# Kernel tuning notes

Measured on AMD Instinct MI355X. Metric: run time of the kernel, lower is better.

## Reference

```python
import jax, jax.numpy as jnp
import numpy as np

N_NODES = 50000
N_EDGES = 800000
IN_DIM = 128
HID = 64
HEADS = 2
OUT_DIM = 2
N_GRAPHS = 512
NEG_SLOPE = 0.2


def setup_inputs() -> dict:
    key = jax.random.key(0)
    ks = jax.random.split(key, 16)
    x = jax.random.normal(ks[0], (N_NODES, IN_DIM), dtype=jnp.float32)
    edge_index = jax.random.randint(ks[1], (2, N_EDGES), 0, N_NODES, dtype=jnp.int64)
    batch = jnp.sort(jax.random.randint(ks[2], (N_NODES,), 0, N_GRAPHS, dtype=jnp.int64))
    s = 0.1
    W1 = jax.random.normal(ks[3], (IN_DIM, HEADS * HID), dtype=jnp.float32) * s
    a_src1 = jax.random.normal(ks[4], (HEADS, HID), dtype=jnp.float32) * s
    a_dst1 = jax.random.normal(ks[5], (HEADS, HID), dtype=jnp.float32) * s
    b1 = jnp.zeros((HEADS * HID,), dtype=jnp.float32)
    W2 = jax.random.normal(ks[6], (HEADS * HID, HID), dtype=jnp.float32) * s
    a_src2 = jax.random.normal(ks[7], (1, HID), dtype=jnp.float32) * s
    a_dst2 = jax.random.normal(ks[8], (1, HID), dtype=jnp.float32) * s
    b2 = jnp.zeros((HID,), dtype=jnp.float32)
    fcW = jax.random.normal(ks[9], (HID, OUT_DIM), dtype=jnp.float32) * s
    fcb = jnp.zeros((OUT_DIM,), dtype=jnp.float32)
    return dict(x=x, edge_index=edge_index, batch=batch,
                W1=W1, a_src1=a_src1, a_dst1=a_dst1, b1=b1,
                W2=W2, a_src2=a_src2, a_dst2=a_dst2, b2=b2,
                fcW=fcW, fcb=fcb)


def gat_layer(x, src, dst, W, a_src, a_dst, b, heads, c_out):
    # x: [N, F] -> h: [N, H, C]
    N = x.shape[0]
    h = (x @ W).reshape(N, heads, c_out)
    alpha_s = jnp.sum(h * a_src, axis=-1)  # [N, H]
    alpha_d = jnp.sum(h * a_dst, axis=-1)  # [N, H]
    e = jax.nn.leaky_relu(alpha_s[src] + alpha_d[dst], NEG_SLOPE)  # [E, H]
    # segment softmax over destination nodes
    emax = jax.ops.segment_max(e, dst, num_segments=N)  # [N, H]
    ex = jnp.exp(e - emax[dst])
    denom = jax.ops.segment_sum(ex, dst, num_segments=N)  # [N, H]
    coef = ex / denom[dst]  # [E, H]
    msg = h[src] * coef[..., None]  # [E, H, C]
    out = jax.ops.segment_sum(msg, dst, num_segments=N)  # [N, H, C]
    return out.reshape(N, heads * c_out) + b


def reference(x, edge_index, batch, W1, a_src1, a_dst1, b1, W2, a_src2, a_dst2, b2, fcW, fcb):
    N = x.shape[0]
    # PyG GATConv add_self_loops=True (shared graph for both layers)
    loops = jnp.arange(N, dtype=edge_index.dtype)
    src = jnp.concatenate([edge_index[0], loops])
    dst = jnp.concatenate([edge_index[1], loops])
    h = jax.nn.relu(gat_layer(x, src, dst, W1, a_src1, a_dst1, b1, HEADS, HID))
    h = jax.nn.relu(gat_layer(h, src, dst, W2, a_src2, a_dst2, b2, 1, HID))
    # global mean pool over graphs
    sums = jax.ops.segment_sum(h, batch, num_segments=N_GRAPHS)  # [G, HID]
    cnts = jax.ops.segment_sum(jnp.ones((N,), dtype=h.dtype), batch, num_segments=N_GRAPHS)
    pooled = sums / jnp.maximum(cnts, 1.0)[:, None]
    logits = pooled @ fcW + fcb
    return jax.nn.log_softmax(logits, axis=1)
```

## Files before the change

### kernel.cpp

```cpp
#include <hip/hip_runtime.h>
#include <math.h>

#define N_NODES 50000
#define N_EDGES 800000
#define EP (N_EDGES + N_NODES)
#define IN_DIM 128
#define HID 64
#define HEADS 2
#define OUT_DIM 2
#define N_GRAPHS 512
#define NEG_SLOPE 0.2f
#define NB_SCAN 196
#define G_GEMM1 1563
#define G_HIST 3321

typedef unsigned int uint;
typedef unsigned short ushort;

__device__ __forceinline__ ushort f2bf(float f) {
    uint u = __float_as_uint(f);
    u += 0x7fffu + ((u >> 16) & 1u);
    return (ushort)(u >> 16);
}
__device__ __forceinline__ float bf_lo(uint u) { return __uint_as_float(u << 16); }
__device__ __forceinline__ float bf_hi(uint u) { return __uint_as_float(u & 0xffff0000u); }

__global__ void fused_gemm1_hist(const float* __restrict__ X, const float* __restrict__ W,
                                 ushort* __restrict__ Y,
                                 const float* __restrict__ a_src, const float* __restrict__ a_dst,
                                 float* __restrict__ as, float* __restrict__ ad,
                                 const int* __restrict__ ei, int* __restrict__ cnt,
                                 int* __restrict__ erank) {
    if (blockIdx.x >= G_GEMM1) {
        int i = (blockIdx.x - G_GEMM1) * 256 + threadIdx.x;
        if (i < EP) {
            int d = (i < N_EDGES) ? ei[N_EDGES + i] : (i - N_EDGES);
            erank[i] = atomicAdd(&cnt[d], 1);
        }
        return;
    }
    __shared__ float xs[32][128];
    const int wave = threadIdx.x >> 6;
    const int lane = threadIdx.x & 63;
    const int base = blockIdx.x * 32 + wave * 8;
    const float4* X4 = (const float4*)X;
    for (int idx = lane; idx < 8 * 32; idx += 64) {
        int r = idx >> 5, c = idx & 31;
        int n = base + r;
        float4 v = (n < N_NODES) ? X4[(size_t)n * 32 + c] : make_float4(0.f, 0.f, 0.f, 0.f);
        ((float4*)xs[wave * 8 + r])[c] = v;
    }
    __syncthreads();

    float acc0[8], acc1[8];
#pragma unroll
    for (int i = 0; i < 8; i++) { acc0[i] = 0.f; acc1[i] = 0.f; }
    for (int k = 0; k < 128; k += 4) {
        float wA[4], wB[4];
#pragma unroll
        for (int kk = 0; kk < 4; kk++) {
            wA[kk] = W[(size_t)(k + kk) * 128 + lane];
            wB[kk] = W[(size_t)(k + kk) * 128 + 64 + lane];
        }
#pragma unroll
        for (int i = 0; i < 8; i++) {
            float4 xv = *(const float4*)&xs[wave * 8 + i][k];
            acc0[i] = fmaf(xv.x, wA[0], acc0[i]); acc1[i] = fmaf(xv.x, wB[0], acc1[i]);
            acc0[i] = fmaf(xv.y, wA[1], acc0[i]); acc1[i] = fmaf(xv.y, wB[1], acc1[i]);
            acc0[i] = fmaf(xv.z, wA[2], acc0[i]); acc1[i] = fmaf(xv.z, wB[2], acc1[i]);
            acc0[i] = fmaf(xv.w, wA[3], acc0[i]); acc1[i] = fmaf(xv.w, wB[3], acc1[i]);
        }
    }

    const float asv0 = a_src[lane],      adv0 = a_dst[lane];
    const float asv1 = a_src[64 + lane], adv1 = a_dst[64 + lane];
#pragma unroll
    for (int i = 0; i < 8; i++) {
        int n = base + i;
        if (n >= N_NODES) continue;
        Y[(size_t)n * 128 + lane]      = f2bf(acc0[i]);
        Y[(size_t)n * 128 + 64 + lane] = f2bf(acc1[i]);
        float s0 = acc0[i] * asv0, d0 = acc0[i] * adv0;
        float s1 = acc1[i] * asv1, d1 = acc1[i] * adv1;
#pragma unroll
        for (int off = 32; off; off >>= 1) {
            s0 += __shfl_xor(s0, off);
            d0 += __shfl_xor(d0, off);
            s1 += __shfl_xor(s1, off);
            d1 += __shfl_xor(d1, off);
        }
        if (lane == 0) {
            as[(size_t)n * 2 + 0] = s0; as[(size_t)n * 2 + 1] = s1;
            ad[(size_t)n * 2 + 0] = d0; ad[(size_t)n * 2 + 1] = d1;
        }
    }
}

__global__ void partial_kernel(const int* __restrict__ cnt, int* __restrict__ bsum) {
    int tid = threadIdx.x;
    int i = blockIdx.x * 256 + tid;
    int lane = tid & 63, wid = tid >> 6;
    int v = (i < N_NODES) ? cnt[i] : 0;
#pragma unroll
    for (int off = 32; off; off >>= 1) v += __shfl_xor(v, off);
    __shared__ int wsum[4];
    if (lane == 0) wsum[wid] = v;
    __syncthreads();
    if (tid == 0) bsum[blockIdx.x] = wsum[0] + wsum[1] + wsum[2] + wsum[3];
}

__global__ void scanb_kernel(const int* __restrict__ bsum, int* __restrict__ boff,
                             int* __restrict__ rowptr) {
    int tid = threadIdx.x;
    int lane = tid & 63, wid = tid >> 6;
    int v = (tid < NB_SCAN) ? bsum[tid] : 0;
    int incl = v;
#pragma unroll
    for (int off = 1; off < 64; off <<= 1) {
        int t = __shfl_up(incl, off);
        if (lane >= off) incl += t;
    }
    __shared__ int wt[4];
    if (lane == 63) wt[wid] = incl;
    __syncthreads();
    int add = 0;
    for (int w = 0; w < wid; w++) add += wt[w];
    incl += add;
    if (tid < NB_SCAN) boff[tid] = incl - v;
    if (tid == NB_SCAN - 1) rowptr[N_NODES] = incl;
}

__global__ void scanc_kernel(const int* __restrict__ cnt, const int* __restrict__ boff,
                             int* __restrict__ rowptr) {
    int tid = threadIdx.x;
    int i = blockIdx.x * 256 + tid;
    int lane = tid & 63, wid = tid >> 6;
    int v = (i < N_NODES) ? cnt[i] : 0;
    int incl = v;
#pragma unroll
    for (int off = 1; off < 64; off <<= 1) {
        int t = __shfl_up(incl, off);
        if (lane >= off) incl += t;
    }
    __shared__ int wt[4];
    if (lane == 63) wt[wid] = incl;
    __syncthreads();
    int add = boff[blockIdx.x];
    for (int w = 0; w < wid; w++) add += wt[w];
    int excl = add + incl - v;
    if (i < N_NODES) rowptr[i] = excl;
}

__global__ void scatter_kernel(const int* __restrict__ ei, const int* __restrict__ rowptr,
                               const int* __restrict__ erank, int* __restrict__ csr_src) {
    int i = blockIdx.x * blockDim.x + threadIdx.x;
    if (i >= EP) return;
    int s, d;
    if (i < N_EDGES) { s = ei[i]; d = ei[N_EDGES + i]; }
    else             { s = d = i - N_EDGES; }
    csr_src[rowptr[d] + erank[i]] = s;
}

__global__ void gemm_alphas2(const float* __restrict__ X, const float* __restrict__ W,
                             ushort* __restrict__ Y,
                             const float* __restrict__ a_src, const float* __restrict__ a_dst,
                             float* __restrict__ as, float* __restrict__ ad, int n_nodes) {
    __shared__ float xs[8][128];
    const int base = blockIdx.x * 8;
    const int t = threadIdx.x;
    const int g = t >> 5, c = t & 31;
    const float4* X4 = (const float4*)X;
    for (int idx = t; idx < 8 * 32; idx += 64) {
        int r = idx >> 5, cc = idx & 31;
        int n = base + r;
        float4 v = (n < n_nodes) ? X4[(size_t)n * 32 + cc] : make_float4(0.f, 0.f, 0.f, 0.f);
        ((float4*)xs[r])[cc] = v;
    }
    __syncthreads();

    float acc0[4], acc1[4];
#pragma unroll
    for (int i = 0; i < 4; i++) { acc0[i] = 0.f; acc1[i] = 0.f; }
    for (int k = 0; k < 128; k += 4) {
        float wA[4], wB[4];
#pragma unroll
        for (int kk = 0; kk < 4; kk++) {
            wA[kk] = W[(size_t)(k + kk) * 64 + c];
            wB[kk] = W[(size_t)(k + kk) * 64 + 32 + c];
        }
#pragma unroll
        for (int i = 0; i < 4; i++) {
            float4 xv = *(const float4*)&xs[g * 4 + i][k];
            acc0[i] = fmaf(xv.x, wA[0], acc0[i]); acc1[i] = fmaf(xv.x, wB[0], acc1[i]);
            acc0[i] = fmaf(xv.y, wA[1], acc0[i]); acc1[i] = fmaf(xv.y, wB[1], acc1[i]);
            acc0[i] = fmaf(xv.z, wA[2], acc0[i]); acc1[i] = fmaf(xv.z, wB[2], acc1[i]);
            acc0[i] = fmaf(xv.w, wA[3], acc0[i]); acc1[i] = fmaf(xv.w, wB[3], acc1[i]);
        }
    }

    const float asvA = a_src[c], asvB = a_src[32 + c];
    const float advA = a_dst[c], advB = a_dst[32 + c];
#pragma unroll
    for (int i = 0; i < 4; i++) {
        int n = base + g * 4 + i;
        if (n >= n_nodes) continue;
        Y[(size_t)n * 64 + c]      = f2bf(acc0[i]);
        Y[(size_t)n * 64 + 32 + c] = f2bf(acc1[i]);
        float s = acc0[i] * asvA + acc1[i] * asvB;
        float d = acc0[i] * advA + acc1[i] * advB;
#pragma unroll
        for (int off = 16; off; off >>= 1) {
            s += __shfl_xor(s, off);
            d += __shfl_xor(d, off);
        }
        if (c == 0) { as[n] = s; ad[n] = d; }
    }
}

__device__ __forceinline__ float lrelu(float e) { return e > 0.f ? e : NEG_SLOPE * e; }

__global__ void node_agg1_kernel(const int* __restrict__ rowptr, const int* __restrict__ csr_src,
                                 const uint* __restrict__ Hb,
                                 const float* __restrict__ as, const float* __restrict__ ad,
                                 const float* __restrict__ b, float* __restrict__ outp) {
    int wave = threadIdx.x >> 6;
    int lane = threadIdx.x & 63;
    int node = blockIdx.x * 4 + wave;
    if (node >= N_NODES) return;
    const int lo = rowptr[node], hi = rowptr[node + 1];
    const float ad0 = ad[(size_t)node * 2 + 0], ad1 = ad[(size_t)node * 2 + 1];

    float exa0 = 0.f, exa1 = 0.f, exb0 = 0.f, exb1 = 0.f;
    int j1 = lo + lane;
    if (j1 < hi) {
        int s = csr_src[j1];
        float2 a = *(const float2*)&as[(size_t)s * 2];
        exa0 = __expf(lrelu(a.x + ad0));
        exa1 = __expf(lrelu(a.y + ad1));
    }
    int j2 = lo + 64 + lane;
    if (j2 < hi) {
        int s = csr_src[j2];
        float2 a = *(const float2*)&as[(size_t)s * 2];
        exb0 = __expf(lrelu(a.x + ad0));
        exb1 = __expf(lrelu(a.y + ad1));
    }
    float d0 = exa0 + exb0, d1 = exa1 + exb1;
    for (int j = lo + 128 + lane; j < hi; j += 64) {
        int s = csr_src[j];
        float2 a = *(const float2*)&as[(size_t)s * 2];
        d0 += __expf(lrelu(a.x + ad0));
        d1 += __expf(lrelu(a.y + ad1));
    }
#pragma unroll
    for (int off = 32; off; off >>= 1) {
        d0 += __shfl_xor(d0, off);
        d1 += __shfl_xor(d1, off);
    }
    const float inv = (lane < 32) ? (1.f / d0) : (1.f / d1);
    const bool h0side = (lane < 32);

    float acc0 = 0.f, acc1 = 0.f;
    const int deg = hi - lo;
    const int n1 = deg < 64 ? deg : 64;
    int j = 0;
    for (; j + 8 <= n1; j += 8) {
        int s0 = csr_src[lo + j + 0], s1 = csr_src[lo + j + 1];
        int s2 = csr_src[lo + j + 2], s3 = csr_src[lo + j + 3];
        int s4 = csr_src[lo + j + 4], s5 = csr_src[lo + j + 5];
        int s6 = csr_src[lo + j + 6], s7 = csr_src[lo + j + 7];
        uint u0 = Hb[(size_t)s0 * 64 + lane];
        uint u1 = Hb[(size_t)s1 * 64 + lane];
        uint u2 = Hb[(size_t)s2 * 64 + lane];
        uint u3 = Hb[(size_t)s3 * 64 + lane];
        uint u4 = Hb[(size_t)s4 * 64 + lane];
        uint u5 = Hb[(size_t)s5 * 64 + lane];
        uint u6 = Hb[(size_t)s6 * 64 + lane];
        uint u7 = Hb[(size_t)s7 * 64 + lane];
        float ca0 = __shfl(exa0, j + 0), cb0 = __shfl(exa1, j + 0);
        float ca1 = __shfl(exa0, j + 1), cb1 = __shfl(exa1, j + 1);
        float ca2 = __shfl(exa0, j + 2), cb2 = __shfl(exa1, j + 2);
        float ca3 = __shfl(exa0, j + 3), cb3 = __shfl(exa1, j + 3);
        float ca4 = __shfl(exa0, j + 4), cb4 = __shfl(exa1, j + 4);
        float ca5 = __shfl(exa0, j + 5), cb5 = __shfl(exa1, j + 5);
        float ca6 = __shfl(exa0, j + 6), cb6 = __shfl(exa1, j + 6);
        float ca7 = __shfl(exa0, j + 7), cb7 = __shfl(exa1, j + 7);
        float c0 = h0side ? ca0 : cb0;
        float c1 = h0side ? ca1 : cb1;
        float c2 = h0side ? ca2 : cb2;
        float c3 = h0side ? ca3 : cb3;
        float c4 = h0side ? ca4 : cb4;
        float c5 = h0side ? ca5 : cb5;
        float c6 = h0side ? ca6 : cb6;
        float c7 = h0side ? ca7 : cb7;
        acc0 = fmaf(bf_lo(u0), c0, acc0); acc1 = fmaf(bf_hi(u0), c0, acc1);
        acc0 = fmaf(bf_lo(u1), c1, acc0); acc1 = fmaf(bf_hi(u1), c1, acc1);
        acc0 = fmaf(bf_lo(u2), c2, acc0); acc1 = fmaf(bf_hi(u2), c2, acc1);
        acc0 = fmaf(bf_lo(u3), c3, acc0); acc1 = fmaf(bf_hi(u3), c3, acc1);
        acc0 = fmaf(bf_lo(u4), c4, acc0); acc1 = fmaf(bf_hi(u4), c4, acc1);
        acc0 = fmaf(bf_lo(u5), c5, acc0); acc1 = fmaf(bf_hi(u5), c5, acc1);
        acc0 = fmaf(bf_lo(u6), c6, acc0); acc1 = fmaf(bf_hi(u6), c6, acc1);
        acc0 = fmaf(bf_lo(u7), c7, acc0); acc1 = fmaf(bf_hi(u7), c7, acc1);
    }
    for (; j < n1; j++) {
        int s = csr_src[lo + j];
        float ca = __shfl(exa0, j), cb = __shfl(exa1, j);
        float c = h0side ? ca : cb;
        uint u = Hb[(size_t)s * 64 + lane];
        acc0 = fmaf(bf_lo(u), c, acc0);
        acc1 = fmaf(bf_hi(u), c, acc1);
    }
    if (deg > 64) {
        const int n2 = deg < 128 ? deg : 128;
        for (j = 64; j < n2; j++) {
            int s = csr_src[lo + j];
            float ca = __shfl(exb0, j - 64), cb = __shfl(exb1, j - 64);
            float c = h0side ? ca : cb;
            uint u = Hb[(size_t)s * 64 + lane];
            acc0 = fmaf(bf_lo(u), c, acc0);
            acc1 = fmaf(bf_hi(u), c, acc1);
        }
        for (int jj = lo + 128; jj < hi; jj++) {
            int s = csr_src[jj];
            float2 a = *(const float2*)&as[(size_t)s * 2];
            float e0 = __expf(lrelu(a.x + ad0));
            float e1 = __expf(lrelu(a.y + ad1));
            float c = h0side ? e0 : e1;
            uint u = Hb[(size_t)s * 64 + lane];
            acc0 = fmaf(bf_lo(u), c, acc0);
            acc1 = fmaf(bf_hi(u), c, acc1);
        }
    }
    float v0 = acc0 * inv + b[2 * lane];
    float v1 = acc1 * inv + b[2 * lane + 1];
    v0 = v0 > 0.f ? v0 : 0.f;
    v1 = v1 > 0.f ? v1 : 0.f;
    *(float2*)&outp[(size_t)node * 128 + 2 * lane] = make_float2(v0, v1);
}

__global__ void node_agg2_kernel(const int* __restrict__ rowptr, const int* __restrict__ csr_src,
                                 const ushort* __restrict__ Hb,
                                 const float* __restrict__ as, const float* __restrict__ ad,
                                 const float* __restrict__ b, float* __restrict__ outp) {
    int wave = threadIdx.x >> 6;
    int lane = threadIdx.x & 63;
    int node = blockIdx.x * 4 + wave;
    if (node >= N_NODES) return;
    const int lo = rowptr[node], hi = rowptr[node + 1];
    const float adN = ad[node];

    float exa = 0.f, exb = 0.f;
    int j1 = lo + lane;
    if (j1 < hi) exa = __expf(lrelu(as[csr_src[j1]] + adN));
    int j2 = lo + 64 + lane;
    if (j2 < hi) exb = __expf(lrelu(as[csr_src[j2]] + adN));
    float d = exa + exb;
    for (int j = lo + 128 + lane; j < hi; j += 64)
        d += __expf(lrelu(as[csr_src[j]] + adN));
#pragma unroll
    for (int off = 32; off; off >>= 1) d += __shfl_xor(d, off);
    const float inv = 1.f / d;

    float acc = 0.f;
    const int deg = hi - lo;
    const int n1 = deg < 64 ? deg : 64;
    int j = 0;
    for (; j + 8 <= n1; j += 8) {
        int s0 = csr_src[lo + j + 0], s1 = csr_src[lo + j + 1];
        int s2 = csr_src[lo + j + 2], s3 = csr_src[lo + j + 3];
        int s4 = csr_src[lo + j + 4], s5 = csr_src[lo + j + 5];
        int s6 = csr_src[lo + j + 6], s7 = csr_src[lo + j + 7];
        float h0 = __uint_as_float(((uint)Hb[(size_t)s0 * 64 + lane]) << 16);
        float h1 = __uint_as_float(((uint)Hb[(size_t)s1 * 64 + lane]) << 16);
        float h2 = __uint_as_float(((uint)Hb[(size_t)s2 * 64 + lane]) << 16);
        float h3 = __uint_as_float(((uint)Hb[(size_t)s3 * 64 + lane]) << 16);
        float h4 = __uint_as_float(((uint)Hb[(size_t)s4 * 64 + lane]) << 16);
        float h5 = __uint_as_float(((uint)Hb[(size_t)s5 * 64 + lane]) << 16);
        float h6 = __uint_as_float(((uint)Hb[(size_t)s6 * 64 + lane]) << 16);
        float h7 = __uint_as_float(((uint)Hb[(size_t)s7 * 64 + lane]) << 16);
        float c0 = __shfl(exa, j + 0), c1 = __shfl(exa, j + 1);
        float c2 = __shfl(exa, j + 2), c3 = __shfl(exa, j + 3);
        float c4 = __shfl(exa, j + 4), c5 = __shfl(exa, j + 5);
        float c6 = __shfl(exa, j + 6), c7 = __shfl(exa, j + 7);
        acc = fmaf(h0, c0, acc);
        acc = fmaf(h1, c1, acc);
        acc = fmaf(h2, c2, acc);
        acc = fmaf(h3, c3, acc);
        acc = fmaf(h4, c4, acc);
        acc = fmaf(h5, c5, acc);
        acc = fmaf(h6, c6, acc);
        acc = fmaf(h7, c7, acc);
    }
    for (; j < n1; j++) {
        float c = __shfl(exa, j);
        acc = fmaf(__uint_as_float(((uint)Hb[(size_t)csr_src[lo + j] * 64 + lane]) << 16), c, acc);
    }
    if (deg > 64) {
        const int n2 = deg < 128 ? deg : 128;
        for (j = 64; j < n2; j++) {
            float c = __shfl(exb, j - 64);
            acc = fmaf(__uint_as_float(((uint)Hb[(size_t)csr_src[lo + j] * 64 + lane]) << 16), c, acc);
        }
        for (int jj = lo + 128; jj < hi; jj++) {
            int s = csr_src[jj];
            float c = __expf(lrelu(as[s] + adN));
            acc = fmaf(__uint_as_float(((uint)Hb[(size_t)s * 64 + lane]) << 16), c, acc);
        }
    }
    float v = acc * inv + b[lane];
    outp[(size_t)node * 64 + lane] = v > 0.f ? v : 0.f;
}

__global__ void pool_fc_kernel(const float* __restrict__ act2,
                               const int* __restrict__ batch,
                               const float* __restrict__ fcW,
                               const float* __restrict__ fcb,
                               float* __restrict__ out) {
    int g = blockIdx.x;
    int tid = threadIdx.x;
    int wid = tid >> 6, c = tid & 63;
    __shared__ int slo, shi;
    if (tid == 0) {
        int lo = 0, hi = N_NODES;
        while (lo < hi) { int m = (lo + hi) >> 1; if (batch[m] < g) lo = m + 1; else hi = m; }
        slo = lo;
        lo = 0; hi = N_NODES;
        while (lo < hi) { int m = (lo + hi) >> 1; if (batch[m] < g + 1) lo = m + 1; else hi = m; }
        shi = lo;
    }
    __syncthreads();
    const int lo = slo, hi = shi;
    float sum = 0.f;
    for (int n = lo + wid; n < hi; n += 4) sum += act2[(size_t)n * HID + c];
    __shared__ float ps[4][HID];
    ps[wid][c] = sum;
    __syncthreads();
    if (wid == 0) {
        float t = ps[0][c] + ps[1][c] + ps[2][c] + ps[3][c];
        float cnt = (float)(hi - lo);
        __shared__ float pooled[HID];
        pooled[c] = t / fmaxf(cnt, 1.f);
        __syncthreads();
        __shared__ float ls[OUT_DIM];
        if (c < OUT_DIM) {
            float l = fcb[c];
#pragma unroll 8
            for (int k = 0; k < HID; k++) l = fmaf(pooled[k], fcW[k * OUT_DIM + c], l);
            ls[c] = l;
        }
        __syncthreads();
        if (c < OUT_DIM) {
            float m = fmaxf(ls[0], ls[1]);
            float lse = m + logf(expf(ls[0] - m) + expf(ls[1] - m));
            out[(size_t)g * OUT_DIM + c] = ls[c] - lse;
        }
    }
}

extern "C" void kernel_launch(void* const* d_in, const int* in_sizes, int n_in,
                              void* d_out, int out_size, void* d_ws, size_t ws_size,
                              hipStream_t stream) {
    const float* x    = (const float*)d_in[0];
    const int*   ei   = (const int*)d_in[1];
    const int*   batch= (const int*)d_in[2];
    const float* W1   = (const float*)d_in[3];
    const float* as1w = (const float*)d_in[4];
    const float* ad1w = (const float*)d_in[5];
    const float* b1   = (const float*)d_in[6];
    const float* W2   = (const float*)d_in[7];
    const float* as2w = (const float*)d_in[8];
    const float* ad2w = (const float*)d_in[9];
    const float* b2   = (const float*)d_in[10];
    const float* fcW  = (const float*)d_in[11];
    const float* fcb  = (const float*)d_in[12];

    const size_t N = N_NODES;
    float* ws = (float*)d_ws;
    ushort* h1b  = (ushort*)ws;
    float* act1  = ws + N * 64;
    ushort* h2b  = (ushort*)(act1 + N * 128);
    float* out2  = act1 + N * 128 + N * 32;
    float* alps1 = out2 + N * 64;
    float* alpd1 = alps1 + N * 2;
    float* alps2 = alpd1 + N * 2;
    float* alpd2 = alps2 + N;
    int* cnt     = (int*)(alpd2 + N);
    int* rowptr  = cnt + N;
    int* bsum    = rowptr + N + 1;
    int* boff    = bsum + NB_SCAN;
    int* erank   = boff + NB_SCAN;
    int* csr_src = erank + EP;

    hipMemsetAsync(cnt, 0, N * sizeof(int), stream);
    fused_gemm1_hist<<<G_GEMM1 + G_HIST, 256, 0, stream>>>(
        x, W1, h1b, as1w, ad1w, alps1, alpd1, ei, cnt, erank);

    partial_kernel<<<NB_SCAN, 256, 0, stream>>>(cnt, bsum);
    scanb_kernel<<<1, 256, 0, stream>>>(bsum, boff, rowptr);
    scanc_kernel<<<NB_SCAN, 256, 0, stream>>>(cnt, boff, rowptr);
    scatter_kernel<<<(EP + 255) / 256, 256, 0, stream>>>(ei, rowptr, erank, csr_src);

    node_agg1_kernel<<<(N + 3) / 4, 256, 0, stream>>>(
        rowptr, csr_src, (const uint*)h1b, alps1, alpd1, b1, act1);

    gemm_alphas2<<<(N + 7) / 8, 64, 0, stream>>>(
        act1, W2, h2b, as2w, ad2w, alps2, alpd2, (int)N);
    node_agg2_kernel<<<(N + 3) / 4, 256, 0, stream>>>(
        rowptr, csr_src, h2b, alps2, alpd2, b2, out2);

    pool_fc_kernel<<<N_GRAPHS, 256, 0, stream>>>(out2, batch, fcW, fcb, (float*)d_out);
}
```

Measured before the change: 291.3 us.

## Fuse layer-2 GEMM and attention logits into layer-1 aggregation kernel

Folds the second-layer linear transform and its source/destination attention dot products into the first-layer aggregation kernel. Each block stages W2 in LDS (32 KB), each wave writes its aggregated 128-wide row to shared memory and computes the 64 outputs directly. This removes the fp32 act1 round trip through global memory and one kernel launch. In exchange, each 512-thread block reloads W2 into LDS, the per-node matvec has low arithmetic reuse, and the large LDS footprint may lower occupancy for the latency-bound gather.

```diff
diff --git a/kernel.cpp b/kernel.cpp
--- a/kernel.cpp
+++ b/kernel.cpp
@@ -161,71 +161,27 @@
     csr_src[rowptr[d] + erank[i]] = s;
 }
 
-__global__ void gemm_alphas2(const float* __restrict__ X, const float* __restrict__ W,
-                             ushort* __restrict__ Y,
-                             const float* __restrict__ a_src, const float* __restrict__ a_dst,
-                             float* __restrict__ as, float* __restrict__ ad, int n_nodes) {
-    __shared__ float xs[8][128];
-    const int base = blockIdx.x * 8;
-    const int t = threadIdx.x;
-    const int g = t >> 5, c = t & 31;
-    const float4* X4 = (const float4*)X;
-    for (int idx = t; idx < 8 * 32; idx += 64) {
-        int r = idx >> 5, cc = idx & 31;
-        int n = base + r;
-        float4 v = (n < n_nodes) ? X4[(size_t)n * 32 + cc] : make_float4(0.f, 0.f, 0.f, 0.f);
-        ((float4*)xs[r])[cc] = v;
-    }
-    __syncthreads();
-
-    float acc0[4], acc1[4];
-#pragma unroll
-    for (int i = 0; i < 4; i++) { acc0[i] = 0.f; acc1[i] = 0.f; }
-    for (int k = 0; k < 128; k += 4) {
-        float wA[4], wB[4];
-#pragma unroll
-        for (int kk = 0; kk < 4; kk++) {
-            wA[kk] = W[(size_t)(k + kk) * 64 + c];
-            wB[kk] = W[(size_t)(k + kk) * 64 + 32 + c];
-        }
-#pragma unroll
-        for (int i = 0; i < 4; i++) {
-            float4 xv = *(const float4*)&xs[g * 4 + i][k];
-            acc0[i] = fmaf(xv.x, wA[0], acc0[i]); acc1[i] = fmaf(xv.x, wB[0], acc1[i]);
-            acc0[i] = fmaf(xv.y, wA[1], acc0[i]); acc1[i] = fmaf(xv.y, wB[1], acc1[i]);
-            acc0[i] = fmaf(xv.z, wA[2], acc0[i]); acc1[i] = fmaf(xv.z, wB[2], acc1[i]);
-            acc0[i] = fmaf(xv.w, wA[3], acc0[i]); acc1[i] = fmaf(xv.w, wB[3], acc1[i]);
-        }
-    }
-
-    const float asvA = a_src[c], asvB = a_src[32 + c];
-    const float advA = a_dst[c], advB = a_dst[32 + c];
-#pragma unroll
-    for (int i = 0; i < 4; i++) {
-        int n = base + g * 4 + i;
-        if (n >= n_nodes) continue;
-        Y[(size_t)n * 64 + c]      = f2bf(acc0[i]);
-        Y[(size_t)n * 64 + 32 + c] = f2bf(acc1[i]);
-        float s = acc0[i] * asvA + acc1[i] * asvB;
-        float d = acc0[i] * advA + acc1[i] * advB;
-#pragma unroll
-        for (int off = 16; off; off >>= 1) {
-            s += __shfl_xor(s, off);
-            d += __shfl_xor(d, off);
-        }
-        if (c == 0) { as[n] = s; ad[n] = d; }
-    }
-}
-
 __device__ __forceinline__ float lrelu(float e) { return e > 0.f ? e : NEG_SLOPE * e; }
 
-__global__ void node_agg1_kernel(const int* __restrict__ rowptr, const int* __restrict__ csr_src,
-                                 const uint* __restrict__ Hb,
-                                 const float* __restrict__ as, const float* __restrict__ ad,
-                                 const float* __restrict__ b, float* __restrict__ outp) {
-    int wave = threadIdx.x >> 6;
-    int lane = threadIdx.x & 63;
-    int node = blockIdx.x * 4 + wave;
+__global__ void __launch_bounds__(512)
+node_agg1_fused(const int* __restrict__ rowptr, const int* __restrict__ csr_src,
+                const uint* __restrict__ Hb,
+                const float* __restrict__ as, const float* __restrict__ ad,
+                const float* __restrict__ b,
+                const float* __restrict__ W2,
+                const float* __restrict__ as2w, const float* __restrict__ ad2w,
+                ushort* __restrict__ Y2, float* __restrict__ as2, float* __restrict__ ad2) {
+    __shared__ float w2s[128 * 64];
+    __shared__ float rowbuf[8][128];
+    const int tid = threadIdx.x;
+    const float4* W24 = (const float4*)W2;
+    for (int idx = tid; idx < 128 * 16; idx += 512)
+        ((float4*)w2s)[idx] = W24[idx];
+    __syncthreads();
+
+    const int wave = tid >> 6;
+    const int lane = tid & 63;
+    const int node = blockIdx.x * 8 + wave;
     if (node >= N_NODES) return;
     const int lo = rowptr[node], hi = rowptr[node + 1];
     const float ad0 = ad[(size_t)node * 2 + 0], ad1 = ad[(size_t)node * 2 + 1];
@@ -335,7 +291,27 @@
     float v1 = acc1 * inv + b[2 * lane + 1];
     v0 = v0 > 0.f ? v0 : 0.f;
     v1 = v1 > 0.f ? v1 : 0.f;
-    *(float2*)&outp[(size_t)node * 128 + 2 * lane] = make_float2(v0, v1);
+
+    rowbuf[wave][2 * lane]     = v0;
+    rowbuf[wave][2 * lane + 1] = v1;
+    float h2c = 0.f;
+#pragma unroll
+    for (int k4 = 0; k4 < 32; k4++) {
+        float4 rv = *(const float4*)&rowbuf[wave][k4 * 4];
+        h2c = fmaf(rv.x, w2s[(k4 * 4 + 0) * 64 + lane], h2c);
+        h2c = fmaf(rv.y, w2s[(k4 * 4 + 1) * 64 + lane], h2c);
+        h2c = fmaf(rv.z, w2s[(k4 * 4 + 2) * 64 + lane], h2c);
+        h2c = fmaf(rv.w, w2s[(k4 * 4 + 3) * 64 + lane], h2c);
+    }
+    Y2[(size_t)node * 64 + lane] = f2bf(h2c);
+    float s2 = h2c * as2w[lane];
+    float d2 = h2c * ad2w[lane];
+#pragma unroll
+    for (int off = 32; off; off >>= 1) {
+        s2 += __shfl_xor(s2, off);
+        d2 += __shfl_xor(d2, off);
+    }
+    if (lane == 0) { as2[node] = s2; ad2[node] = d2; }
 }
 
 __global__ void node_agg2_kernel(const int* __restrict__ rowptr, const int* __restrict__ csr_src,
@@ -477,9 +453,8 @@
     const size_t N = N_NODES;
     float* ws = (float*)d_ws;
     ushort* h1b  = (ushort*)ws;
-    float* act1  = ws + N * 64;
-    ushort* h2b  = (ushort*)(act1 + N * 128);
-    float* out2  = act1 + N * 128 + N * 32;
+    ushort* h2b  = (ushort*)(ws + N * 64);
+    float* out2  = ws + N * 64 + N * 32;
     float* alps1 = out2 + N * 64;
     float* alpd1 = alps1 + N * 2;
     float* alps2 = alpd1 + N * 2;
@@ -500,11 +475,10 @@
     scanc_kernel<<<NB_SCAN, 256, 0, stream>>>(cnt, boff, rowptr);
     scatter_kernel<<<(EP + 255) / 256, 256, 0, stream>>>(ei, rowptr, erank, csr_src);
 
-    node_agg1_kernel<<<(N + 3) / 4, 256, 0, stream>>>(
-        rowptr, csr_src, (const uint*)h1b, alps1, alpd1, b1, act1);
-
-    gemm_alphas2<<<(N + 7) / 8, 64, 0, stream>>>(
-        act1, W2, h2b, as2w, ad2w, alps2, alpd2, (int)N);
+    node_agg1_fused<<<(N + 7) / 8, 512, 0, stream>>>(
+        rowptr, csr_src, (const uint*)h1b, alps1, alpd1, b1,
+        W2, as2w, ad2w, h2b, alps2, alpd2);
+
     node_agg2_kernel<<<(N + 3) / 4, 256, 0, stream>>>(
         rowptr, csr_src, h2b, alps2, alpd2, b2, out2);
 
```

Result: slower. 309.0 us (+6.1%).

## Split GEMM1 across histogram and scatter kernels and fold block-scan into scanc

Applied to the files above, without the earlier changes.

The layer-1 GEMM is split into two halves. One half runs alongside the degree-histogram atomics and the other alongside the CSR scatter, so memory-bound atomic and scatter work overlaps with compute in both launches. The single-block scan of block sums is merged into the per-block scan kernel: each block redundantly scans the 196 partial sums itself, which removes a launch and the boff buffer. This trades two fewer launches for some redundant scan work per block and a less even block mix in each fused launch.

```diff
diff --git a/kernel.cpp b/kernel.cpp
--- a/kernel.cpp
+++ b/kernel.cpp
@@ -11,8 +11,11 @@
 #define N_GRAPHS 512
 #define NEG_SLOPE 0.2f
 #define NB_SCAN 196
-#define G_GEMM1 1563
+#define GA_GEMM 782
+#define GB_GEMM 781
+#define GB_BASE 25024
 #define G_HIST 3321
+#define G_SCAT 3321
 
 typedef unsigned int uint;
 typedef unsigned short ushort;
@@ -24,25 +27,18 @@
 }
 __device__ __forceinline__ float bf_lo(uint u) { return __uint_as_float(u << 16); }
 __device__ __forceinline__ float bf_hi(uint u) { return __uint_as_float(u & 0xffff0000u); }
-
-__global__ void fused_gemm1_hist(const float* __restrict__ X, const float* __restrict__ W,
-                                 ushort* __restrict__ Y,
-                                 const float* __restrict__ a_src, const float* __restrict__ a_dst,
-                                 float* __restrict__ as, float* __restrict__ ad,
-                                 const int* __restrict__ ei, int* __restrict__ cnt,
-                                 int* __restrict__ erank) {
-    if (blockIdx.x >= G_GEMM1) {
-        int i = (blockIdx.x - G_GEMM1) * 256 + threadIdx.x;
-        if (i < EP) {
-            int d = (i < N_EDGES) ? ei[N_EDGES + i] : (i - N_EDGES);
-            erank[i] = atomicAdd(&cnt[d], 1);
-        }
-        return;
-    }
-    __shared__ float xs[32][128];
+__device__ __forceinline__ float lrelu(float e) { return e > 0.f ? e : NEG_SLOPE * e; }
+
+__device__ __forceinline__ void gemm1_block(float (*xs)[128], int base_block,
+                                            const float* __restrict__ X,
+                                            const float* __restrict__ W,
+                                            ushort* __restrict__ Y,
+                                            const float* __restrict__ a_src,
+                                            const float* __restrict__ a_dst,
+                                            float* __restrict__ as, float* __restrict__ ad) {
     const int wave = threadIdx.x >> 6;
     const int lane = threadIdx.x & 63;
-    const int base = blockIdx.x * 32 + wave * 8;
+    const int base = base_block + wave * 8;
     const float4* X4 = (const float4*)X;
     for (int idx = lane; idx < 8 * 32; idx += 64) {
         int r = idx >> 5, c = idx & 31;
@@ -96,6 +92,44 @@
     }
 }
 
+__global__ void fused_gemm1a_hist(const float* __restrict__ X, const float* __restrict__ W,
+                                  ushort* __restrict__ Y,
+                                  const float* __restrict__ a_src, const float* __restrict__ a_dst,
+                                  float* __restrict__ as, float* __restrict__ ad,
+                                  const int* __restrict__ ei, int* __restrict__ cnt,
+                                  int* __restrict__ erank) {
+    __shared__ float xs[32][128];
+    if (blockIdx.x >= GA_GEMM) {
+        int i = (blockIdx.x - GA_GEMM) * 256 + threadIdx.x;
+        if (i < EP) {
+            int d = (i < N_EDGES) ? ei[N_EDGES + i] : (i - N_EDGES);
+            erank[i] = atomicAdd(&cnt[d], 1);
+        }
+        return;
+    }
+    gemm1_block(xs, blockIdx.x * 32, X, W, Y, a_src, a_dst, as, ad);
+}
+
+__global__ void fused_gemm1b_scatter(const float* __restrict__ X, const float* __restrict__ W,
+                                     ushort* __restrict__ Y,
+                                     const float* __restrict__ a_src, const float* __restrict__ a_dst,
+                                     float* __restrict__ as, float* __restrict__ ad,
+                                     const int* __restrict__ ei, const int* __restrict__ rowptr,
+                                     const int* __restrict__ erank, int* __restrict__ csr_src) {
+    __shared__ float xs[32][128];
+    if (blockIdx.x >= GB_GEMM) {
+        int i = (blockIdx.x - GB_GEMM) * 256 + threadIdx.x;
+        if (i < EP) {
+            int s, d;
+            if (i < N_EDGES) { s = ei[i]; d = ei[N_EDGES + i]; }
+            else             { s = d = i - N_EDGES; }
+            csr_src[rowptr[d] + erank[i]] = s;
+        }
+        return;
+    }
+    gemm1_block(xs, GB_BASE + blockIdx.x * 32, X, W, Y, a_src, a_dst, as, ad);
+}
+
 __global__ void partial_kernel(const int* __restrict__ cnt, int* __restrict__ bsum) {
     int tid = threadIdx.x;
     int i = blockIdx.x * 256 + tid;
@@ -109,56 +143,41 @@
     if (tid == 0) bsum[blockIdx.x] = wsum[0] + wsum[1] + wsum[2] + wsum[3];
 }
 
-__global__ void scanb_kernel(const int* __restrict__ bsum, int* __restrict__ boff,
+__global__ void scanc_kernel(const int* __restrict__ cnt, const int* __restrict__ bsum,
                              int* __restrict__ rowptr) {
     int tid = threadIdx.x;
     int lane = tid & 63, wid = tid >> 6;
-    int v = (tid < NB_SCAN) ? bsum[tid] : 0;
+    __shared__ int wtA[4], wtB[4];
+    __shared__ int s_boff;
+
+    int bv = (tid < NB_SCAN) ? bsum[tid] : 0;
+    int bincl = bv;
+#pragma unroll
+    for (int off = 1; off < 64; off <<= 1) {
+        int t = __shfl_up(bincl, off);
+        if (lane >= off) bincl += t;
+    }
+    if (lane == 63) wtA[wid] = bincl;
+    __syncthreads();
+    int addA = 0;
+    for (int w = 0; w < wid; w++) addA += wtA[w];
+    bincl += addA;
+    if (tid == blockIdx.x) s_boff = bincl - bv;
+    if (blockIdx.x == 0 && tid == NB_SCAN - 1) rowptr[N_NODES] = bincl;
+
+    int i = blockIdx.x * 256 + tid;
+    int v = (i < N_NODES) ? cnt[i] : 0;
     int incl = v;
 #pragma unroll
     for (int off = 1; off < 64; off <<= 1) {
         int t = __shfl_up(incl, off);
         if (lane >= off) incl += t;
     }
-    __shared__ int wt[4];
-    if (lane == 63) wt[wid] = incl;
-    __syncthreads();
-    int add = 0;
-    for (int w = 0; w < wid; w++) add += wt[w];
-    incl += add;
-    if (tid < NB_SCAN) boff[tid] = incl - v;
-    if (tid == NB_SCAN - 1) rowptr[N_NODES] = incl;
-}
-
-__global__ void scanc_kernel(const int* __restrict__ cnt, const int* __restrict__ boff,
-                             int* __restrict__ rowptr) {
-    int tid = threadIdx.x;
-    int i = blockIdx.x * 256 + tid;
-    int lane = tid & 63, wid = tid >> 6;
-    int v = (i < N_NODES) ? cnt[i] : 0;
-    int incl = v;
-#pragma unroll
-    for (int off = 1; off < 64; off <<= 1) {
-        int t = __shfl_up(incl, off);
-        if (lane >= off) incl += t;
-    }
-    __shared__ int wt[4];
-    if (lane == 63) wt[wid] = incl;
-    __syncthreads();
-    int add = boff[blockIdx.x];
-    for (int w = 0; w < wid; w++) add += wt[w];
-    int excl = add + incl - v;
-    if (i < N_NODES) rowptr[i] = excl;
-}
-
-__global__ void scatter_kernel(const int* __restrict__ ei, const int* __restrict__ rowptr,
-                               const int* __restrict__ erank, int* __restrict__ csr_src) {
-    int i = blockIdx.x * blockDim.x + threadIdx.x;
-    if (i >= EP) return;
-    int s, d;
-    if (i < N_EDGES) { s = ei[i]; d = ei[N_EDGES + i]; }
-    else             { s = d = i - N_EDGES; }
-    csr_src[rowptr[d] + erank[i]] = s;
+    if (lane == 63) wtB[wid] = incl;
+    __syncthreads();
+    int add = s_boff;
+    for (int w = 0; w < wid; w++) add += wtB[w];
+    if (i < N_NODES) rowptr[i] = add + incl - v;
 }
 
 __global__ void gemm_alphas2(const float* __restrict__ X, const float* __restrict__ W,
@@ -216,8 +235,6 @@
         if (c == 0) { as[n] = s; ad[n] = d; }
     }
 }
-
-__device__ __forceinline__ float lrelu(float e) { return e > 0.f ? e : NEG_SLOPE * e; }
 
 __global__ void node_agg1_kernel(const int* __restrict__ rowptr, const int* __restrict__ csr_src,
                                  const uint* __restrict__ Hb,
@@ -487,18 +504,18 @@
     int* cnt     = (int*)(alpd2 + N);
     int* rowptr  = cnt + N;
     int* bsum    = rowptr + N + 1;
-    int* boff    = bsum + NB_SCAN;
-    int* erank   = boff + NB_SCAN;
+    int* erank   = bsum + NB_SCAN;
     int* csr_src = erank + EP;
 
     hipMemsetAsync(cnt, 0, N * sizeof(int), stream);
-    fused_gemm1_hist<<<G_GEMM1 + G_HIST, 256, 0, stream>>>(
+    fused_gemm1a_hist<<<GA_GEMM + G_HIST, 256, 0, stream>>>(
         x, W1, h1b, as1w, ad1w, alps1, alpd1, ei, cnt, erank);
 
     partial_kernel<<<NB_SCAN, 256, 0, stream>>>(cnt, bsum);
-    scanb_kernel<<<1, 256, 0, stream>>>(bsum, boff, rowptr);
-    scanc_kernel<<<NB_SCAN, 256, 0, stream>>>(cnt, boff, rowptr);
-    scatter_kernel<<<(EP + 255) / 256, 256, 0, stream>>>(ei, rowptr, erank, csr_src);
+    scanc_kernel<<<NB_SCAN, 256, 0, stream>>>(cnt, bsum, rowptr);
+
+    fused_gemm1b_scatter<<<GB_GEMM + G_SCAT, 256, 0, stream>>>(
+        x, W1, h1b, as1w, ad1w, alps1, alpd1, ei, rowptr, erank, csr_src);
 
     node_agg1_kernel<<<(N + 3) / 4, 256, 0, stream>>>(
         rowptr, csr_src, (const uint*)h1b, alps1, alpd1, b1, act1);
```

Result: slower. 307.1 us (+5.4%).
